# Kernel tuning notes

Hardware: AMD Instinct MI355X
Metric: run time of the kernel (lower is better)

Reference implementation:

```python
import jax, jax.numpy as jnp
import numpy as np

N = 50000      # nodes across all enclosing subgraphs
E = 1200000    # edges
R = 5          # num_relations
NB = 2         # num_bases
D = 64         # num_features == latent_dim per layer
L = 4          # num_layers
B = 1024       # num enclosing subgraphs (one user + one movie each)


def setup_inputs() -> dict:
    key = jax.random.key(0)
    ks = jax.random.split(key, 10)
    # one-hot node-label features; first B nodes are target users (x[:,0]==1),
    # next B nodes are target movies (x[:,1]==1)
    labels = jax.random.randint(ks[0], (N,), 2, D)
    x = jax.nn.one_hot(labels, D, dtype=jnp.float32)
    x = x.at[:B, :].set(0.0).at[:B, 0].set(1.0)
    x = x.at[B:2 * B, :].set(0.0).at[B:2 * B, 1].set(1.0)
    src = jax.random.randint(ks[1], (E,), 0, N)
    dst = jax.random.randint(ks[2], (E,), 0, N)
    etype = jax.random.randint(ks[3], (E,), 0, R)
    s = 1.0 / np.sqrt(D)
    basis = jax.random.normal(ks[4], (L, NB, D, D), dtype=jnp.float32) * s
    comp = jax.random.normal(ks[5], (L, R, NB), dtype=jnp.float32) * s
    root = jax.random.normal(ks[6], (L, D, D), dtype=jnp.float32) * s
    bias = jnp.zeros((L, D), dtype=jnp.float32)
    w1 = jax.random.normal(ks[7], (2 * L * D, 128), dtype=jnp.float32) * (1.0 / np.sqrt(2 * L * D))
    b1 = jnp.zeros((128,), dtype=jnp.float32)
    w2 = jax.random.normal(ks[8], (128, 1), dtype=jnp.float32) * (1.0 / np.sqrt(128))
    b2 = jnp.zeros((1,), dtype=jnp.float32)
    return dict(x=x, basis=basis, comp=comp, root=root, bias=bias,
                w1=w1, b1=b1, w2=w2, b2=b2,
                src=src, dst=dst, etype=etype, num_graphs=B)


def _rgcn(h, src, dst, etype, basis_l, comp_l, root_l, bias_l):
    # PyG RGCNConv with basis decomposition and per-relation mean aggregation.
    n_rel = comp_l.shape[0]
    x_src = h[src]                                # [E, Din] gather
    w_e = comp_l[etype]                           # [E, NB] basis coefficients per edge
    msg = jnp.zeros((src.shape[0], basis_l.shape[-1]), h.dtype)
    for b in range(basis_l.shape[0]):             # NB = 2, fixed small loop
        msg = msg + w_e[:, b:b + 1] * (x_src @ basis_l[b])
    # mean over incoming edges per (dst, relation)
    seg = dst * n_rel + etype
    cnt = jax.ops.segment_sum(jnp.ones((src.shape[0],), h.dtype), seg,
                              num_segments=h.shape[0] * n_rel)
    msg = msg * (1.0 / jnp.maximum(cnt[seg], 1.0))[:, None]
    agg = jax.ops.segment_sum(msg, dst, num_segments=h.shape[0])  # scatter-add
    return agg + h @ root_l + bias_l


def reference(x, basis, comp, root, bias, w1, b1, w2, b2, src, dst, etype, num_graphs):
    h = x
    states = []
    for l in range(basis.shape[0]):               # 4 layers
        h = jnp.tanh(_rgcn(h, src, dst, etype, basis[l], comp[l], root[l], bias[l]))
        states.append(h)
    cat = jnp.concatenate(states, axis=1)         # [N, L*D]
    users = jnp.nonzero(x[:, 0] == 1.0, size=num_graphs)[0]
    movies = jnp.nonzero(x[:, 1] == 1.0, size=num_graphs)[0]
    g = jnp.concatenate([cat[users], cat[movies]], axis=1)  # [B, 2*L*D]
    hid = jax.nn.relu(g @ w1 + b1)                # eval mode: dropout is a no-op
    out = hid @ w2 + b2
    return out[:, 0]
```

## Files before the change

### kernel.cpp

```cpp
#include <hip/hip_runtime.h>
#include <hip/hip_fp16.h>
#include <math.h>

#define D      64
#define L      4
#define R      5
#define BGRAPH 1024
#define CT     4096
#define BK     128
#define INVCAP 8192

typedef __attribute__((ext_vector_type(8))) short short8;
typedef __attribute__((ext_vector_type(8))) _Float16 half8;
typedef __attribute__((ext_vector_type(4))) float f32x4;


__global__ void hist_init_k(const int* __restrict__ dst, int* __restrict__ bh,
                            const float* __restrict__ x, __half* __restrict__ hf,
                            unsigned char* __restrict__ labels,
                            const float* __restrict__ basis, const float* __restrict__ root,
                            ushort* __restrict__ Mhi, ushort* __restrict__ Mlo,
                            int E, int nbl, int nbuck, int N, int nbCopy) {
    if ((int)blockIdx.x < nbl) {
        __shared__ int cnt[392];
        for (int k = threadIdx.x; k < nbuck; k += 256) cnt[k] = 0;
        __syncthreads();
        int base = blockIdx.x * CT;
        int end = base + CT < E ? base + CT : E;
        for (int i = base + threadIdx.x; i < end; i += 256)
            atomicAdd(&cnt[dst[i] >> 7], 1);
        __syncthreads();
        for (int k = threadIdx.x; k < nbuck; k += 256)
            bh[k * nbl + blockIdx.x] = cnt[k];
    } else if ((int)blockIdx.x < nbl + nbCopy) {
        int wid = threadIdx.x >> 6, lane = threadIdx.x & 63;
        int v = (blockIdx.x - nbl) * 4 + wid;
        if (v >= N) return;
        float val = x[(size_t)v * D + lane];
        hf[(size_t)v * D + lane] = __float2half(val);
        unsigned long long m = __ballot(val > 0.5f);
        if (lane == 0) labels[v] = (unsigned char)__builtin_ctzll(m);
    } else {
        int t = (blockIdx.x - nbl - nbCopy) * 256 + threadIdx.x;
        if (t >= L * 4 * 6 * 64 * 8) return;
        int j = t & 7;
        int lane = (t >> 3) & 63;
        int rem = t >> 9;
        int kt = rem % 6;
        int lcg = rem / 6;
        int cg = lcg & 3, l = lcg >> 2;
        int k = kt * 32 + (lane >> 4) * 8 + j;
        int col = cg * 16 + (lane & 15);
        float val;
        if (k < 64)       val = basis[(((size_t)l * 2 + 0) * D + k) * D + col];
        else if (k < 128) val = basis[(((size_t)l * 2 + 1) * D + (k - 64)) * D + col];
        else              val = root[((size_t)l * D + (k - 128)) * D + col];
        __half hi = __float2half(val);
        Mhi[t] = __half_as_ushort(hi);
        Mlo[t] = __half_as_ushort(__float2half(val - __half2float(hi)));
    }
}

__global__ void scan1(const int* __restrict__ hist, int* __restrict__ offs,
                      int* __restrict__ bsums, int n) {
    __shared__ int tmp[256];
    int i = blockIdx.x * 256 + threadIdx.x;
    int v = (i < n) ? hist[i] : 0;
    tmp[threadIdx.x] = v;
    __syncthreads();
    for (int o = 1; o < 256; o <<= 1) {
        int t = 0;
        if (threadIdx.x >= o) t = tmp[threadIdx.x - o];
        __syncthreads();
        if (threadIdx.x >= o) tmp[threadIdx.x] += t;
        __syncthreads();
    }
    if (i < n) offs[i] = tmp[threadIdx.x] - v;
    if (threadIdx.x == 255) bsums[blockIdx.x] = tmp[255];
}

__device__ __forceinline__ void scan_bsums(const int* __restrict__ bsums, int nb,
                                           int* tmp, int* ex) {
    int t = threadIdx.x;
    int v = (t < nb) ? bsums[t] : 0;
    tmp[t] = v;
    __syncthreads();
    for (int o = 1; o < 512; o <<= 1) {
        int tv = 0;
        if (t >= o) tv = tmp[t - o];
        __syncthreads();
        if (t >= o) tmp[t] += tv;
        __syncthreads();
    }
    ex[t] = tmp[t] - v;
    __syncthreads();
}

__global__ __launch_bounds__(512)
void coarse_scatter(const int* __restrict__ dst, const int* __restrict__ src,
                    const int* __restrict__ et, const int* __restrict__ bh,
                    const int* __restrict__ bsums, int* __restrict__ pe,
                    int E, int nbl, int nbuck, int nb) {
    __shared__ int tmp[512];
    __shared__ int ex[512];
    __shared__ int cur[392];
    scan_bsums(bsums, nb, tmp, ex);
    for (int k = threadIdx.x; k < nbuck; k += 512) {
        int idx = k * nbl + blockIdx.x;
        cur[k] = bh[idx] + ex[idx >> 8];
    }
    __syncthreads();
    int base = blockIdx.x * CT;
    int end = base + CT < E ? base + CT : E;
    for (int i = base + threadIdx.x; i < end; i += 512) {
        int d = dst[i];
        int pos = atomicAdd(&cur[d >> 7], 1);
        pe[pos] = src[i] | (et[i] << 16) | ((d & 127) << 19);
    }
}

__global__ __launch_bounds__(512)
void fine_sort(const int* __restrict__ pe, const int* __restrict__ bh,
               const int* __restrict__ bsums, int* __restrict__ offs,
               int* __restrict__ meta, float* __restrict__ invcN,
               int E, int nbl, int N, int nb) {
    __shared__ int tmp[512];
    __shared__ int ex[512];
    __shared__ int cnt[BK];
    __shared__ int pref[BK];
    __shared__ int cur[BK];
    __shared__ int cntR[BK * R];
    __shared__ int inv[INVCAP];
    int b = blockIdx.x, t = threadIdx.x;
    scan_bsums(bsums, nb, tmp, ex);
    int i0 = b * nbl;
    int rbeg = bh[i0] + ex[i0 >> 8];
    int rend;
    if (b == gridDim.x - 1) rend = E;
    else { int i1 = (b + 1) * nbl; rend = bh[i1] + ex[i1 >> 8]; }
    int sz = rend - rbeg;
    if (t < BK) { cnt[t] = 0; cur[t] = 0; }
    for (int k = t; k < BK * R; k += 512) cntR[k] = 0;
    __syncthreads();
    for (int i = rbeg + t; i < rend; i += 512) {
        int pk = pe[i];
        int ln = (pk >> 19) & 127;
        atomicAdd(&cnt[ln], 1);
        atomicAdd(&cntR[ln * R + ((pk >> 16) & 7)], 1);
    }
    __syncthreads();
    if (t < BK) pref[t] = cnt[t];
    __syncthreads();
    for (int o = 1; o < BK; o <<= 1) {
        int tv = 0;
        if (t >= o && t < BK) tv = pref[t - o];
        __syncthreads();
        if (t >= o && t < BK) pref[t] += tv;
        __syncthreads();
    }
    if (t < BK) {
        int node = b * BK + t;
        if (node <= N) offs[node] = rbeg + pref[t] - cnt[t];
    }
    for (int k = t; k < BK * R; k += 512) {
        int c = cntR[k];
        float ic = 1.0f / (float)(c > 0 ? c : 1);
        ((float*)cntR)[k] = ic;
        int node = b * BK + k / R;
        if (node < N) invcN[(size_t)b * BK * R + k] = ic;
    }
    __syncthreads();
    if (sz <= INVCAP) {
        for (int i = rbeg + t; i < rend; i += 512) {
            int pk = pe[i];
            int ln = (pk >> 19) & 127;
            int lp = pref[ln] - cnt[ln] + atomicAdd(&cur[ln], 1);
            inv[lp] = pk;
        }
        __syncthreads();
        for (int k = t; k < sz; k += 512)
            meta[rbeg + k] = inv[k] & 0x7FFFF;
    } else {
        for (int i = rbeg + t; i < rend; i += 512) {
            int pk = pe[i];
            int ln = (pk >> 19) & 127;
            int pos = rbeg + (pref[ln] - cnt[ln]) + atomicAdd(&cur[ln], 1);
            meta[pos] = pk & 0x7FFFF;
        }
    }
}

__global__ __launch_bounds__(256)
void gather0_k(const int* __restrict__ offs, const int* __restrict__ meta,
               const float* __restrict__ invcN, const unsigned char* __restrict__ labels,
               const float* __restrict__ comp_l, __half* __restrict__ Z, int N) {
    __shared__ float zl[16][128];
    __shared__ float2 wnT[16][5];
    int tid = threadIdx.x;
    int vbase0 = blockIdx.x * 16;
    if (tid < 16 * R) {
        int n = tid / R, r = tid % R;
        int v = vbase0 + n;
        float ic = (v < N) ? invcN[(size_t)v * R + r] : 0.f;
        wnT[n][r] = make_float2(comp_l[2 * r] * ic, comp_l[2 * r + 1] * ic);
    }
    for (int k = tid; k < 16 * 128; k += 256) ((float*)zl)[k] = 0.f;
    __syncthreads();
    int nl = tid >> 4, sl = tid & 15;
    int v = vbase0 + nl;
    if (v < N) {
        int b = offs[v], e2 = offs[v + 1];
        for (int i = b + sl; i < e2; i += 16) {
            int pk = meta[i];
            int s = pk & 0xFFFF;
            int r = (pk >> 16) & 7;
            float2 wt = wnT[nl][r];
            int lab = labels[s];
            atomicAdd(&zl[nl][lab], wt.x);
            atomicAdd(&zl[nl][64 + lab], wt.y);
        }
    }
    __syncthreads();
    {
        int idx = tid * 8;
        int n = idx >> 7, c = idx & 127;
        int v2 = vbase0 + n;
        if (v2 < N) {
            union { short8 v8; __half h[8]; } o;
            #pragma unroll
            for (int j = 0; j < 8; ++j) o.h[j] = __float2half(zl[n][c + j]);
            *(short8*)(Z + (size_t)v2 * 128 + c) = o.v8;
        }
    }
}

__global__ __launch_bounds__(256)
void gather_k(const int* __restrict__ offs, const int* __restrict__ meta,
              const float* __restrict__ invcN, const __half* __restrict__ hfin,
              const float* __restrict__ comp_l, __half* __restrict__ Z, int N) {
    __shared__ float2 wnT[16][5];
    int tid = threadIdx.x;
    int vbase0 = blockIdx.x * 16;
    if (tid < 16 * R) {
        int n = tid / R, r = tid % R;
        int v = vbase0 + n;
        float ic = (v < N) ? invcN[(size_t)v * R + r] : 0.f;
        wnT[n][r] = make_float2(comp_l[2 * r] * ic, comp_l[2 * r + 1] * ic);
    }
    __syncthreads();

    int wid = tid >> 6, lane = tid & 63;
    int h = lane >> 5;
    int n = (lane >> 3) & 3;
    int q = lane & 7;
    int nl = wid * 4 + n;
    int v = vbase0 + nl;
    bool vlive = v < N;
    int vc = vlive ? v : 0;
    int b = offs[vc];
    int e2 = vlive ? offs[vc + 1] : b;
    int len = e2 - b;
    int lmax = len;
    lmax = max(lmax, __shfl_xor(lmax, 8));
    lmax = max(lmax, __shfl_xor(lmax, 16));
    int nits = (lmax + 1) >> 1;

    float s0[8] = {0,0,0,0,0,0,0,0}, s1[8] = {0,0,0,0,0,0,0,0};
    const float4* hf16 = (const float4*)hfin;
    #pragma unroll 4
    for (int it = 0; it < nits; ++it) {
        int e = it * 2 + h;
        bool live = e < len;
        int gi = live ? (b + e) : 0;
        int pk = meta[gi];
        int s = pk & 0xFFFF;
        int r = (pk >> 16) & 7;
        float2 wt = wnT[nl][r];
        float w0 = live ? wt.x : 0.f;
        float w1 = live ? wt.y : 0.f;
        float4 hv = hf16[(size_t)s * 8 + q];
        const __half2* hp = (const __half2*)&hv;
        #pragma unroll
        for (int k2 = 0; k2 < 4; ++k2) {
            float lo = __low2float(hp[k2]), hi = __high2float(hp[k2]);
            s0[2 * k2]     = fmaf(w0, lo, s0[2 * k2]);
            s0[2 * k2 + 1] = fmaf(w0, hi, s0[2 * k2 + 1]);
            s1[2 * k2]     = fmaf(w1, lo, s1[2 * k2]);
            s1[2 * k2 + 1] = fmaf(w1, hi, s1[2 * k2 + 1]);
        }
    }
    #pragma unroll
    for (int k = 0; k < 8; ++k) {
        s0[k] += __shfl_xor(s0[k], 32);
        s1[k] += __shfl_xor(s1[k], 32);
    }
    if (vlive && h == 0) {
        union { short8 v8; __half h[8]; } o0, o1;
        #pragma unroll
        for (int k = 0; k < 8; ++k) {
            o0.h[k] = __float2half(s0[k]);
            o1.h[k] = __float2half(s1[k]);
        }
        *(short8*)(Z + (size_t)v * 128 + 8 * q)      = o0.v8;
        *(short8*)(Z + (size_t)v * 128 + 64 + 8 * q) = o1.v8;
    }
}

__global__ __launch_bounds__(256)
void transform_k(const __half* __restrict__ Z, const __half* __restrict__ hfin,
                 const ushort* __restrict__ Mhi_l, const ushort* __restrict__ Mlo_l,
                 const float* __restrict__ bias_l, __half* __restrict__ hfout,
                 float* __restrict__ g, int l, int N) {
    int wid = threadIdx.x >> 6, lane = threadIdx.x & 63;
    int tile = blockIdx.x * 4 + wid;
    if (tile * 16 >= N) return;
    int m = lane & 15, lg = lane >> 4;
    int row = tile * 16 + m;
    int rowc = row < N ? row : N - 1;

    half8 a[6];
    #pragma unroll
    for (int kt = 0; kt < 6; ++kt) {
        const __half* hp = (kt < 4)
            ? Z    + (size_t)rowc * 128 + kt * 32 + lg * 8
            : hfin + (size_t)rowc * D + (kt - 4) * 32 + lg * 8;
        a[kt] = *(const half8*)hp;
    }

    #pragma unroll
    for (int cg = 0; cg < 4; ++cg) {
        int col = cg * 16 + m;
        float bv = bias_l[col];
        f32x4 acc = { bv, bv, bv, bv };
        #pragma unroll
        for (int kt = 0; kt < 6; ++kt) {
            size_t boff = ((size_t)(cg * 6 + kt) * 64 + lane) * 8;
            half8 bhi = *(const half8*)(Mhi_l + boff);
            half8 blo = *(const half8*)(Mlo_l + boff);
            acc = __builtin_amdgcn_mfma_f32_16x16x32_f16(a[kt], bhi, acc, 0, 0, 0);
            acc = __builtin_amdgcn_mfma_f32_16x16x32_f16(a[kt], blo, acc, 0, 0, 0);
        }
        int rowbase = tile * 16 + lg * 4;
        #pragma unroll
        for (int r = 0; r < 4; ++r) {
            int node = rowbase + r;
            if (node < N) {
                float tv = tanhf(acc[r]);
                hfout[(size_t)node * D + col] = __float2half(tv);
                if (node < BGRAPH)
                    g[(size_t)node * (2 * L * D) + l * D + col] = tv;
                else if (node < 2 * BGRAPH)
                    g[(size_t)(node - BGRAPH) * (2 * L * D) + L * D + l * D + col] = tv;
            }
        }
    }
}

__global__ void mlp4(const float* __restrict__ g, const float* __restrict__ w1,
                     const float* __restrict__ b1, const float* __restrict__ w2,
                     const float* __restrict__ b2, float* __restrict__ out) {
    __shared__ float gl[4][512];
    __shared__ float red[2][4][128];
    int tid = threadIdx.x;
    int rowbase = blockIdx.x * 4;
    for (int i = tid; i < 4 * 512; i += 256)
        gl[i >> 9][i & 511] = g[(size_t)rowbase * 512 + i];
    __syncthreads();
    int t = tid & 127, kh = tid >> 7;
    float s0 = 0.f, s1 = 0.f, s2 = 0.f, s3 = 0.f;
    int k0 = kh * 256;
    #pragma unroll 4
    for (int k = k0; k < k0 + 256; ++k) {
        float wv = w1[k * 128 + t];
        s0 = fmaf(gl[0][k], wv, s0);
        s1 = fmaf(gl[1][k], wv, s1);
        s2 = fmaf(gl[2][k], wv, s2);
        s3 = fmaf(gl[3][k], wv, s3);
    }
    red[kh][0][t] = s0; red[kh][1][t] = s1; red[kh][2][t] = s2; red[kh][3][t] = s3;
    __syncthreads();
    if (kh == 0) {
        #pragma unroll
        for (int r = 0; r < 4; ++r)
            gl[r][t] = fmaxf(red[0][r][t] + red[1][r][t] + b1[t], 0.f) * w2[t];
    }
    __syncthreads();
    int w = tid >> 6, lane = tid & 63;
    float val = gl[w][lane] + gl[w][lane + 64];
    #pragma unroll
    for (int o = 32; o > 0; o >>= 1) val += __shfl_down(val, o);
    if (lane == 0) out[rowbase + w] = val + b2[0];
}

extern "C" void kernel_launch(void* const* d_in, const int* in_sizes, int n_in,
                              void* d_out, int out_size, void* d_ws, size_t ws_size,
                              hipStream_t stream) {
    const float* x     = (const float*)d_in[0];
    const float* basis = (const float*)d_in[1];
    const float* comp  = (const float*)d_in[2];
    const float* root  = (const float*)d_in[3];
    const float* bias  = (const float*)d_in[4];
    const float* w1    = (const float*)d_in[5];
    const float* b1    = (const float*)d_in[6];
    const float* w2    = (const float*)d_in[7];
    const float* b2    = (const float*)d_in[8];
    const int*   src   = (const int*)d_in[9];
    const int*   dst   = (const int*)d_in[10];
    const int*   et    = (const int*)d_in[11];
    float* out = (float*)d_out;

    const int N = in_sizes[0] / D;
    const int E = in_sizes[9];

    const int nbl = (E + CT - 1) / CT;
    const int nbuck = (N + BK - 1) / BK;
    const int nbh = nbuck * nbl;
    const int nb = (nbh + 255) / 256;

    char* p = (char*)d_ws;
    auto alloc = [&](size_t bytes) -> char* {
        char* q = p;
        p += (bytes + 255) & ~(size_t)255;
        return q;
    };
    int*    offsN = (int*)alloc((size_t)(N + 1) * 4);
    int*    bh    = (int*)alloc((size_t)(nbh + 1) * 4);
    int*    bsums = (int*)alloc(1024 * 4);
    int*    pe    = (int*)alloc((size_t)E * 4);
    int*    meta  = (int*)alloc((size_t)E * 4);
    float*  invcN = (float*)alloc((size_t)(nbuck * BK) * R * 4);
    unsigned char* labels = (unsigned char*)alloc((size_t)N);
    __half* Z     = (__half*)alloc((size_t)N * 128 * 2);
    __half* hf0   = (__half*)alloc((size_t)N * D * 2);
    __half* hf1   = (__half*)alloc((size_t)N * D * 2);
    float*  gbuf  = (float*)alloc((size_t)BGRAPH * 2 * L * D * 4);
    ushort* Mhi   = (ushort*)alloc((size_t)L * 4 * 6 * 64 * 8 * 2);
    ushort* Mlo   = (ushort*)alloc((size_t)L * 4 * 6 * 64 * 8 * 2);

    int nbCopy = (N + 3) / 4;
    hist_init_k<<<nbl + nbCopy + 192, 256, 0, stream>>>(
        dst, bh, x, hf0, labels, basis, root, Mhi, Mlo, E, nbl, nbuck, N, nbCopy);
    scan1<<<nb, 256, 0, stream>>>(bh, bh, bsums, nbh);
    coarse_scatter<<<nbl, 512, 0, stream>>>(dst, src, et, bh, bsums, pe,
                                            E, nbl, nbuck, nb);
    fine_sort<<<nbuck, 512, 0, stream>>>(pe, bh, bsums, offsN, meta, invcN,
                                         E, nbl, N, nb);

    __half* hbuf[2] = { hf0, hf1 };
    int g0grid = (N + 15) / 16;
    int ggrid = (N + 15) / 16;
    int tgrid = ((N + 15) / 16 + 3) / 4;
    for (int l = 0; l < L; ++l) {
        if (l == 0)
            gather0_k<<<g0grid, 256, 0, stream>>>(offsN, meta, invcN, labels,
                                                  comp, Z, N);
        else
            gather_k<<<ggrid, 256, 0, stream>>>(offsN, meta, invcN, hbuf[l & 1],
                                                comp + (size_t)l * R * 2, Z, N);
        transform_k<<<tgrid, 256, 0, stream>>>(Z, hbuf[l & 1],
                                               Mhi + (size_t)l * 4 * 6 * 64 * 8,
                                               Mlo + (size_t)l * 4 * 6 * 64 * 8,
                                               bias + (size_t)l * D,
                                               hbuf[(l + 1) & 1], gbuf, l, N);
    }
    mlp4<<<BGRAPH / 4, 256, 0, stream>>>(gbuf, w1, b1, w2, b2, out);
}
```

Baseline: 193.2 us.

## Fuse per-layer gather and MFMA transform into one kernel via shared memory

Merges the gather (edge aggregation) and transform (MFMA matmul + tanh) kernels into a single per-layer kernel. The 16-node aggregated tile is kept in shared memory instead of being written to and read back from a global Z buffer, which removes that buffer and halves the kernel launches per layer. Each of the 4 waves now computes one 16-column group of the tile rather than one wave doing all 4, which changes how the work is split across waves and adds a block-wide sync between the two phases.

```diff
diff --git a/kernel.cpp b/kernel.cpp
--- a/kernel.cpp
+++ b/kernel.cpp
@@ -191,167 +191,148 @@
 }
 
 __global__ __launch_bounds__(256)
-void gather0_k(const int* __restrict__ offs, const int* __restrict__ meta,
-               const float* __restrict__ invcN, const unsigned char* __restrict__ labels,
-               const float* __restrict__ comp_l, __half* __restrict__ Z, int N) {
-    __shared__ float zl[16][128];
+void layer_fused(const int* __restrict__ offs, const int* __restrict__ meta,
+                 const float* __restrict__ invcN, const unsigned char* __restrict__ labels,
+                 const __half* __restrict__ hfin,
+                 const ushort* __restrict__ Mhi_l, const ushort* __restrict__ Mlo_l,
+                 const float* __restrict__ bias_l, const float* __restrict__ comp_l,
+                 __half* __restrict__ hfout, float* __restrict__ g, int l, int N) {
+    __shared__ union {
+        float  f32[16][132];
+        __half f16[16][136];
+    } zu;
     __shared__ float2 wnT[16][5];
     int tid = threadIdx.x;
-    int vbase0 = blockIdx.x * 16;
+    int tile = blockIdx.x;
+    int vbase0 = tile * 16;
     if (tid < 16 * R) {
         int n = tid / R, r = tid % R;
         int v = vbase0 + n;
         float ic = (v < N) ? invcN[(size_t)v * R + r] : 0.f;
         wnT[n][r] = make_float2(comp_l[2 * r] * ic, comp_l[2 * r + 1] * ic);
     }
-    for (int k = tid; k < 16 * 128; k += 256) ((float*)zl)[k] = 0.f;
-    __syncthreads();
-    int nl = tid >> 4, sl = tid & 15;
-    int v = vbase0 + nl;
-    if (v < N) {
-        int b = offs[v], e2 = offs[v + 1];
-        for (int i = b + sl; i < e2; i += 16) {
-            int pk = meta[i];
+    int wid = tid >> 6, lane = tid & 63;
+
+    if (l == 0) {
+        for (int k = tid; k < 16 * 132; k += 256) ((float*)zu.f32)[k] = 0.f;
+        __syncthreads();
+        int nl = tid >> 4, sl = tid & 15;
+        int v = vbase0 + nl;
+        if (v < N) {
+            int b = offs[v], e2 = offs[v + 1];
+            for (int i = b + sl; i < e2; i += 16) {
+                int pk = meta[i];
+                int s = pk & 0xFFFF;
+                int r = (pk >> 16) & 7;
+                float2 wt = wnT[nl][r];
+                int lab = labels[s];
+                atomicAdd(&zu.f32[nl][lab], wt.x);
+                atomicAdd(&zu.f32[nl][64 + lab], wt.y);
+            }
+        }
+    } else {
+        __syncthreads();
+        int h = lane >> 5;
+        int n = (lane >> 3) & 3;
+        int q = lane & 7;
+        int nl = wid * 4 + n;
+        int v = vbase0 + nl;
+        bool vlive = v < N;
+        int vc = vlive ? v : 0;
+        int b = offs[vc];
+        int e2 = vlive ? offs[vc + 1] : b;
+        int len = e2 - b;
+        int lmax = len;
+        lmax = max(lmax, __shfl_xor(lmax, 8));
+        lmax = max(lmax, __shfl_xor(lmax, 16));
+        int nits = (lmax + 1) >> 1;
+        float s0[8] = {0,0,0,0,0,0,0,0}, s1[8] = {0,0,0,0,0,0,0,0};
+        const float4* hf16 = (const float4*)hfin;
+        #pragma unroll 4
+        for (int it = 0; it < nits; ++it) {
+            int e = it * 2 + h;
+            bool live = e < len;
+            int gi = live ? (b + e) : 0;
+            int pk = meta[gi];
             int s = pk & 0xFFFF;
             int r = (pk >> 16) & 7;
             float2 wt = wnT[nl][r];
-            int lab = labels[s];
-            atomicAdd(&zl[nl][lab], wt.x);
-            atomicAdd(&zl[nl][64 + lab], wt.y);
-        }
-    }
-    __syncthreads();
-    {
-        int idx = tid * 8;
-        int n = idx >> 7, c = idx & 127;
-        int v2 = vbase0 + n;
-        if (v2 < N) {
-            union { short8 v8; __half h[8]; } o;
+            float w0 = live ? wt.x : 0.f;
+            float w1 = live ? wt.y : 0.f;
+            float4 hv = hf16[(size_t)s * 8 + q];
+            const __half2* hp = (const __half2*)&hv;
             #pragma unroll
-            for (int j = 0; j < 8; ++j) o.h[j] = __float2half(zl[n][c + j]);
-            *(short8*)(Z + (size_t)v2 * 128 + c) = o.v8;
-        }
-    }
-}
-
-__global__ __launch_bounds__(256)
-void gather_k(const int* __restrict__ offs, const int* __restrict__ meta,
-              const float* __restrict__ invcN, const __half* __restrict__ hfin,
-              const float* __restrict__ comp_l, __half* __restrict__ Z, int N) {
-    __shared__ float2 wnT[16][5];
-    int tid = threadIdx.x;
-    int vbase0 = blockIdx.x * 16;
-    if (tid < 16 * R) {
-        int n = tid / R, r = tid % R;
-        int v = vbase0 + n;
-        float ic = (v < N) ? invcN[(size_t)v * R + r] : 0.f;
-        wnT[n][r] = make_float2(comp_l[2 * r] * ic, comp_l[2 * r + 1] * ic);
-    }
-    __syncthreads();
-
-    int wid = tid >> 6, lane = tid & 63;
-    int h = lane >> 5;
-    int n = (lane >> 3) & 3;
-    int q = lane & 7;
-    int nl = wid * 4 + n;
-    int v = vbase0 + nl;
-    bool vlive = v < N;
-    int vc = vlive ? v : 0;
-    int b = offs[vc];
-    int e2 = vlive ? offs[vc + 1] : b;
-    int len = e2 - b;
-    int lmax = len;
-    lmax = max(lmax, __shfl_xor(lmax, 8));
-    lmax = max(lmax, __shfl_xor(lmax, 16));
-    int nits = (lmax + 1) >> 1;
-
-    float s0[8] = {0,0,0,0,0,0,0,0}, s1[8] = {0,0,0,0,0,0,0,0};
-    const float4* hf16 = (const float4*)hfin;
-    #pragma unroll 4
-    for (int it = 0; it < nits; ++it) {
-        int e = it * 2 + h;
-        bool live = e < len;
-        int gi = live ? (b + e) : 0;
-        int pk = meta[gi];
-        int s = pk & 0xFFFF;
-        int r = (pk >> 16) & 7;
-        float2 wt = wnT[nl][r];
-        float w0 = live ? wt.x : 0.f;
-        float w1 = live ? wt.y : 0.f;
-        float4 hv = hf16[(size_t)s * 8 + q];
-        const __half2* hp = (const __half2*)&hv;
-        #pragma unroll
-        for (int k2 = 0; k2 < 4; ++k2) {
-            float lo = __low2float(hp[k2]), hi = __high2float(hp[k2]);
-            s0[2 * k2]     = fmaf(w0, lo, s0[2 * k2]);
-            s0[2 * k2 + 1] = fmaf(w0, hi, s0[2 * k2 + 1]);
-            s1[2 * k2]     = fmaf(w1, lo, s1[2 * k2]);
-            s1[2 * k2 + 1] = fmaf(w1, hi, s1[2 * k2 + 1]);
-        }
-    }
-    #pragma unroll
-    for (int k = 0; k < 8; ++k) {
-        s0[k] += __shfl_xor(s0[k], 32);
-        s1[k] += __shfl_xor(s1[k], 32);
-    }
-    if (vlive && h == 0) {
-        union { short8 v8; __half h[8]; } o0, o1;
+            for (int k2 = 0; k2 < 4; ++k2) {
+                float lo = __low2float(hp[k2]), hi = __high2float(hp[k2]);
+                s0[2 * k2]     = fmaf(w0, lo, s0[2 * k2]);
+                s0[2 * k2 + 1] = fmaf(w0, hi, s0[2 * k2 + 1]);
+                s1[2 * k2]     = fmaf(w1, lo, s1[2 * k2]);
+                s1[2 * k2 + 1] = fmaf(w1, hi, s1[2 * k2 + 1]);
+            }
+        }
         #pragma unroll
         for (int k = 0; k < 8; ++k) {
-            o0.h[k] = __float2half(s0[k]);
-            o1.h[k] = __float2half(s1[k]);
-        }
-        *(short8*)(Z + (size_t)v * 128 + 8 * q)      = o0.v8;
-        *(short8*)(Z + (size_t)v * 128 + 64 + 8 * q) = o1.v8;
-    }
-}
-
-__global__ __launch_bounds__(256)
-void transform_k(const __half* __restrict__ Z, const __half* __restrict__ hfin,
-                 const ushort* __restrict__ Mhi_l, const ushort* __restrict__ Mlo_l,
-                 const float* __restrict__ bias_l, __half* __restrict__ hfout,
-                 float* __restrict__ g, int l, int N) {
-    int wid = threadIdx.x >> 6, lane = threadIdx.x & 63;
-    int tile = blockIdx.x * 4 + wid;
-    if (tile * 16 >= N) return;
+            s0[k] += __shfl_xor(s0[k], 32);
+            s1[k] += __shfl_xor(s1[k], 32);
+        }
+        if (vlive && h == 0) {
+            union { short8 v8; __half hh[8]; } o0, o1;
+            #pragma unroll
+            for (int k = 0; k < 8; ++k) {
+                o0.hh[k] = __float2half(s0[k]);
+                o1.hh[k] = __float2half(s1[k]);
+            }
+            *(short8*)(&zu.f16[nl][8 * q])      = o0.v8;
+            *(short8*)(&zu.f16[nl][64 + 8 * q]) = o1.v8;
+        }
+    }
+    __syncthreads();
+
     int m = lane & 15, lg = lane >> 4;
-    int row = tile * 16 + m;
+    int row = vbase0 + m;
     int rowc = row < N ? row : N - 1;
-
     half8 a[6];
+    if (l == 0) {
+        #pragma unroll
+        for (int kt = 0; kt < 4; ++kt) {
+            const float* zp = &zu.f32[m][kt * 32 + lg * 8];
+            union { half8 v; __half hh[8]; } A;
+            #pragma unroll
+            for (int q2 = 0; q2 < 8; ++q2) A.hh[q2] = __float2half(zp[q2]);
+            a[kt] = A.v;
+        }
+    } else {
+        #pragma unroll
+        for (int kt = 0; kt < 4; ++kt)
+            a[kt] = *(const half8*)(&zu.f16[m][kt * 32 + lg * 8]);
+    }
+    #pragma unroll
+    for (int kt = 4; kt < 6; ++kt)
+        a[kt] = *(const half8*)(hfin + (size_t)rowc * D + (kt - 4) * 32 + lg * 8);
+
+    int cg = wid;
+    int col = cg * 16 + m;
+    float bv = bias_l[col];
+    f32x4 acc = { bv, bv, bv, bv };
     #pragma unroll
     for (int kt = 0; kt < 6; ++kt) {
-        const __half* hp = (kt < 4)
-            ? Z    + (size_t)rowc * 128 + kt * 32 + lg * 8
-            : hfin + (size_t)rowc * D + (kt - 4) * 32 + lg * 8;
-        a[kt] = *(const half8*)hp;
-    }
-
+        size_t boff = ((size_t)(cg * 6 + kt) * 64 + lane) * 8;
+        half8 bhi = *(const half8*)(Mhi_l + boff);
+        half8 blo = *(const half8*)(Mlo_l + boff);
+        acc = __builtin_amdgcn_mfma_f32_16x16x32_f16(a[kt], bhi, acc, 0, 0, 0);
+        acc = __builtin_amdgcn_mfma_f32_16x16x32_f16(a[kt], blo, acc, 0, 0, 0);
+    }
+    int rowbase = vbase0 + lg * 4;
     #pragma unroll
-    for (int cg = 0; cg < 4; ++cg) {
-        int col = cg * 16 + m;
-        float bv = bias_l[col];
-        f32x4 acc = { bv, bv, bv, bv };
-        #pragma unroll
-        for (int kt = 0; kt < 6; ++kt) {
-            size_t boff = ((size_t)(cg * 6 + kt) * 64 + lane) * 8;
-            half8 bhi = *(const half8*)(Mhi_l + boff);
-            half8 blo = *(const half8*)(Mlo_l + boff);
-            acc = __builtin_amdgcn_mfma_f32_16x16x32_f16(a[kt], bhi, acc, 0, 0, 0);
-            acc = __builtin_amdgcn_mfma_f32_16x16x32_f16(a[kt], blo, acc, 0, 0, 0);
-        }
-        int rowbase = tile * 16 + lg * 4;
-        #pragma unroll
-        for (int r = 0; r < 4; ++r) {
-            int node = rowbase + r;
-            if (node < N) {
-                float tv = tanhf(acc[r]);
-                hfout[(size_t)node * D + col] = __float2half(tv);
-                if (node < BGRAPH)
-                    g[(size_t)node * (2 * L * D) + l * D + col] = tv;
-                else if (node < 2 * BGRAPH)
-                    g[(size_t)(node - BGRAPH) * (2 * L * D) + L * D + l * D + col] = tv;
-            }
+    for (int r = 0; r < 4; ++r) {
+        int node = rowbase + r;
+        if (node < N) {
+            float tv = tanhf(acc[r]);
+            hfout[(size_t)node * D + col] = __float2half(tv);
+            if (node < BGRAPH)
+                g[(size_t)node * (2 * L * D) + l * D + col] = tv;
+            else if (node < 2 * BGRAPH)
+                g[(size_t)(node - BGRAPH) * (2 * L * D) + L * D + l * D + col] = tv;
         }
     }
 }
@@ -430,7 +411,6 @@
     int*    meta  = (int*)alloc((size_t)E * 4);
     float*  invcN = (float*)alloc((size_t)(nbuck * BK) * R * 4);
     unsigned char* labels = (unsigned char*)alloc((size_t)N);
-    __half* Z     = (__half*)alloc((size_t)N * 128 * 2);
     __half* hf0   = (__half*)alloc((size_t)N * D * 2);
     __half* hf1   = (__half*)alloc((size_t)N * D * 2);
     float*  gbuf  = (float*)alloc((size_t)BGRAPH * 2 * L * D * 4);
@@ -447,20 +427,14 @@
                                          E, nbl, N, nb);
 
     __half* hbuf[2] = { hf0, hf1 };
-    int g0grid = (N + 15) / 16;
-    int ggrid = (N + 15) / 16;
-    int tgrid = ((N + 15) / 16 + 3) / 4;
+    int lgrid = (N + 15) / 16;
     for (int l = 0; l < L; ++l) {
-        if (l == 0)
-            gather0_k<<<g0grid, 256, 0, stream>>>(offsN, meta, invcN, labels,
-                                                  comp, Z, N);
-        else
-            gather_k<<<ggrid, 256, 0, stream>>>(offsN, meta, invcN, hbuf[l & 1],
-                                                comp + (size_t)l * R * 2, Z, N);
-        transform_k<<<tgrid, 256, 0, stream>>>(Z, hbuf[l & 1],
+        layer_fused<<<lgrid, 256, 0, stream>>>(offsN, meta, invcN, labels,
+                                               hbuf[l & 1],
                                                Mhi + (size_t)l * 4 * 6 * 64 * 8,
                                                Mlo + (size_t)l * 4 * 6 * 64 * 8,
                                                bias + (size_t)l * D,
+                                               comp + (size_t)l * R * 2,
                                                hbuf[(l + 1) & 1], gbuf, l, N);
     }
     mlp4<<<BGRAPH / 4, 256, 0, stream>>>(gbuf, w1, b1, w2, b2, out);
```

New measurement: 172.9 us. 1.12x faster.
